# Optimization experiments

Hardware: AMD Instinct MI355X
Metric: run time of the kernel (lower is better)

Reference implementation:

```python
import jax, jax.numpy as jnp
import numpy as np

NUM_HEADS = 16
GROUP_SIZE = 4
RMS_EPS = 1e-6


def _rope_cos_sin(S, head_dim):
    # matches compute_freqs_cis: freqs = 1/10000**(arange(0,hd,2)/hd), angles = outer(t, freqs)
    inv_freq = 1.0 / (10000.0 ** (jnp.arange(0, head_dim, 2, dtype=jnp.float32) / head_dim))
    t = jnp.arange(S, dtype=jnp.float32)
    angles = t[:, None] * inv_freq[None, :]          # [S, hd/2]
    return jnp.cos(angles), jnp.sin(angles)


def _apply_rope(x, cos, sin):
    # x: [B, S, h, hd]; complex multiply on (even, odd) pairs
    B, S, h, hd = x.shape
    xr = x.reshape(B, S, h, hd // 2, 2)
    x0, x1 = xr[..., 0], xr[..., 1]
    c = cos[None, :, None, :]
    s = sin[None, :, None, :]
    o0 = x0 * c - x1 * s
    o1 = x0 * s + x1 * c
    return jnp.stack([o0, o1], axis=-1).reshape(B, S, h, hd)


def setup_inputs() -> dict:
    key = jax.random.key(0)
    k1, k2, k3 = jax.random.split(key, 3)
    B, S, H = 4, 2048, 2048
    g = GROUP_SIZE
    x = jax.random.normal(k1, (B, S, H), dtype=jnp.float32)
    w_attn = jax.random.normal(k2, (H, H + 2 * H // g), dtype=jnp.float32) * 0.02
    w_proj = jax.random.normal(k3, (H, H), dtype=jnp.float32) * 0.02
    norm_w = jnp.ones((H,), dtype=jnp.float32)
    return {"x": x, "w_attn": w_attn, "w_proj": w_proj, "norm_w": norm_w}


def reference(x, w_attn, w_proj, norm_w):
    B, S, H = x.shape
    nh = NUM_HEADS
    g = GROUP_SIZE
    nkv = nh // g
    hd = H // nh
    ghd = H // g

    qkv = jnp.einsum('bsh,hf->bsf', x, w_attn)
    q = qkv[..., :H].reshape(B, S, nh, hd)
    k = qkv[..., H:H + ghd].reshape(B, S, nkv, hd)
    v = qkv[..., H + ghd:].reshape(B, S, nkv, hd)

    cos, sin = _rope_cos_sin(S, hd)
    q = _apply_rope(q, cos, sin)
    k = _apply_rope(k, cos, sin)

    q = q.transpose(0, 2, 1, 3)                      # [B, nh, S, hd]
    k = jnp.repeat(k.transpose(0, 2, 1, 3), g, axis=1)   # [B, nh, S, hd]
    v = jnp.repeat(v.transpose(0, 2, 1, 3), g, axis=1)

    scale = 1.0 / jnp.sqrt(jnp.float32(hd))
    scores = jnp.einsum('bhqd,bhkd->bhqk', q, k) * scale
    causal = jnp.tril(jnp.ones((S, S), dtype=bool))
    scores = jnp.where(causal[None, None], scores, jnp.finfo(scores.dtype).min)
    attn = jax.nn.softmax(scores, axis=-1)
    y = jnp.einsum('bhqk,bhkd->bhqd', attn, v)       # [B, nh, S, hd]
    y = y.transpose(0, 2, 1, 3).reshape(B, S, H)

    y = jnp.einsum('bsh,ho->bso', y, w_proj)
    # RMSNorm
    rms = jnp.sqrt(jnp.mean(jnp.square(y), axis=-1, keepdims=True) + RMS_EPS)
    return (y / rms) * norm_w
```

## Files before the change

kernel.cpp:

```cpp
#include <hip/hip_runtime.h>

#define DEVI __device__ __forceinline__

using u16 = unsigned short;
using u32 = unsigned int;

typedef __attribute__((ext_vector_type(8))) short short8v;
typedef __attribute__((ext_vector_type(4))) float f32x4;
typedef __attribute__((ext_vector_type(2))) u32 u32x2;

DEVI u16 f2b(float f) {
  u32 u = __builtin_bit_cast(u32, f);
  u += 0x7fffu + ((u >> 16) & 1u);
  return (u16)(u >> 16);
}
DEVI float b2f(u16 b) { return __builtin_bit_cast(float, (u32)b << 16); }

DEVI void gload16(const void* g, void* l) {
  __builtin_amdgcn_global_load_lds(
      (const __attribute__((address_space(1))) void*)g,
      (__attribute__((address_space(3))) void*)l, 16, 0, 0);
}

__global__ __launch_bounds__(256) void cvt_x_k(const float* __restrict__ in,
                                               u16* __restrict__ out) {
  size_t i = ((size_t)blockIdx.x * 256 + threadIdx.x) * 8;
  f32x4 a = *(const f32x4*)(in + i);
  f32x4 c = *(const f32x4*)(in + i + 4);
  short8v o;
  o[0] = (short)f2b(a[0]); o[1] = (short)f2b(a[1]);
  o[2] = (short)f2b(a[2]); o[3] = (short)f2b(a[3]);
  o[4] = (short)f2b(c[0]); o[5] = (short)f2b(c[1]);
  o[6] = (short)f2b(c[2]); o[7] = (short)f2b(c[3]);
  *(short8v*)(out + i) = o;
}

__global__ __launch_bounds__(256) void transpose_cvt_k(
    const float* __restrict__ in, u16* __restrict__ out, int R, int Ccols) {
  __shared__ u16 tile[64][65];
  const int r0 = blockIdx.y * 64, c0 = blockIdx.x * 64;
  const int tx = threadIdx.x & 63, ty = threadIdx.x >> 6;
#pragma unroll
  for (int jj = 0; jj < 16; ++jj) {
    int r = ty + jj * 4;
    tile[r][tx] = f2b(in[(size_t)(r0 + r) * Ccols + c0 + tx]);
  }
  __syncthreads();
#pragma unroll
  for (int jj = 0; jj < 16; ++jj) {
    int c = ty + jj * 4;
    out[(size_t)(c0 + c) * R + r0 + tx] = tile[tx][c];
  }
}

__global__ __launch_bounds__(256) void rope_table_k(float* __restrict__ cosT,
                                                    float* __restrict__ sinT) {
  int idx = blockIdx.x * 256 + threadIdx.x;
  int s = idx >> 6, i = idx & 63;
  float inv_freq = expf(-(float)i * (1.0f / 64.0f) * 9.210340371976184f);
  float ang = (float)s * inv_freq;
  cosT[idx] = cosf(ang);
  sinT[idx] = sinf(ang);
}

__global__ __launch_bounds__(256) void rope_scatter_k(
    const u16* __restrict__ qkv, const float* __restrict__ cosT,
    const float* __restrict__ sinT, u16* __restrict__ q_r,
    u16* __restrict__ k_r) {
  const float QS = 0.08838834764831845f * 1.4426950408889634f;
  const int row = blockIdx.x;
  const int b = row >> 11, s = row & 2047;
  const u16* in = qkv + (size_t)row * 3072;
  const float* cp = cosT + s * 64;
  const float* sp = sinT + s * 64;
  for (int p = threadIdx.x; p < 1280; p += 256) {
    int f0 = p * 2;
    u32 pair = *(const u32*)(in + f0);
    float x0 = b2f((u16)(pair & 0xffffu));
    float x1 = b2f((u16)(pair >> 16));
    int d, head;
    u16* dst;
    bool isq = (f0 < 2048);
    if (isq) {
      head = f0 >> 7; d = f0 & 127;
      dst = q_r + (((size_t)(b * 16 + head)) * 2048 + s) * 128 + d;
    } else {
      int idx = f0 - 2048;
      head = idx >> 7; d = idx & 127;
      dst = k_r + (((size_t)(b * 4 + head)) * 2048 + s) * 128 + d;
    }
    int i = d >> 1;
    float c = cp[i], sn = sp[i];
    float o0 = x0 * c - x1 * sn;
    float o1 = x0 * sn + x1 * c;
    if (isq) { o0 *= QS; o1 *= QS; }
    *(u32*)dst = (u32)f2b(o0) | ((u32)f2b(o1) << 16);
  }
}

__global__ __launch_bounds__(256) void v_trans_k(const u16* __restrict__ qkv,
                                                 u16* __restrict__ vT) {
  __shared__ u16 tile[64][65];
  const int s0 = blockIdx.x * 64, d0 = blockIdx.y * 64;
  const int bk = blockIdx.z;
  const int b = bk >> 2, kh = bk & 3;
  const int tx = threadIdx.x & 63, ty = threadIdx.x >> 6;
  const u16* src = qkv + ((size_t)b * 2048) * 3072 + 2560 + kh * 128;
#pragma unroll
  for (int jj = 0; jj < 16; ++jj) {
    int s = ty + jj * 4;
    tile[s][tx] = src[(size_t)(s0 + s) * 3072 + d0 + tx];
  }
  __syncthreads();
  u16* dst = vT + (((size_t)bk * 128 + d0) * 2048) + s0;
#pragma unroll
  for (int jj = 0; jj < 16; ++jj) {
    int dd = ty + jj * 4;
    dst[(size_t)dd * 2048 + tx] = tile[tx][dd];
  }
}

DEVI short8v ldf(const char* half, int r, int slot) {
  return *(const short8v*)(half + r * 64 + (((slot) ^ (r & 3)) << 4));
}

DEVI void stg(const u16* __restrict__ G, int row0, int Kd, int T, int kh,
              char* dst, int t, int w) {
#pragma unroll
  for (int i = 0; i < 2; ++i) {
    int off = i * 8192 + t * 16;
    int r = off >> 6;
    int gs = ((off >> 4) & 3) ^ (r & 3);
    gload16((const char*)G +
                (((size_t)(row0 + r) * Kd) + T * 64 + kh * 32 + gs * 8) * 2,
            dst + i * 8192 + w * 1024);
  }
}

#define VM4 asm volatile("s_waitcnt vmcnt(4)" ::: "memory")
#define PH(P2, KS, CH, STAGE_STMT, TAILWAIT)                                   \
  {                                                                            \
    if ((CH) == 0) {                                                           \
      _Pragma("unroll") for (int mt = 0; mt < 8; ++mt) af[mt] =                \
          ldf(Ab + (P2) * 32768 + (KS) * 16384, wm * 128 + mt * 16 + lo, hi);  \
    }                                                                          \
    bf0 = ldf(Bb + (P2) * 32768 + (KS) * 16384, wn * 64 + (CH) * 32 + lo, hi);\
    bf1 = ldf(Bb + (P2) * 32768 + (KS) * 16384,                                \
              wn * 64 + (CH) * 32 + 16 + lo, hi);                              \
    STAGE_STMT;                                                                \
    __builtin_amdgcn_sched_barrier(0);                                         \
    __builtin_amdgcn_s_barrier();                                              \
    asm volatile("s_waitcnt lgkmcnt(0)" ::: "memory");                         \
    __builtin_amdgcn_sched_barrier(0);                                         \
    __builtin_amdgcn_s_setprio(1);                                             \
    _Pragma("unroll") for (int mt = 0; mt < 8; ++mt) {                         \
      acc[mt][(CH) * 2] = __builtin_amdgcn_mfma_f32_16x16x32_bf16(             \
          af[mt], bf0, acc[mt][(CH) * 2], 0, 0, 0);                            \
      acc[mt][(CH) * 2 + 1] = __builtin_amdgcn_mfma_f32_16x16x32_bf16(         \
          af[mt], bf1, acc[mt][(CH) * 2 + 1], 0, 0, 0);                        \
    }                                                                          \
    __builtin_amdgcn_s_setprio(0);                                             \
    TAILWAIT;                                                                  \
    __builtin_amdgcn_sched_barrier(0);                                         \
    __builtin_amdgcn_s_barrier();                                              \
    __builtin_amdgcn_sched_barrier(0);                                         \
  }

__global__ __launch_bounds__(512, 2) void gemm256_k(const u16* __restrict__ A,
                                                    const u16* __restrict__ BT,
                                                    u16* __restrict__ C, int N,
                                                    int Kd) {
  __shared__ __align__(16) char lds[131072];
  char* Ab = lds;
  char* Bb = lds + 65536;

  const int t = threadIdx.x;
  const int lane = t & 63, lo = lane & 15, hi = lane >> 4;
  const int w = t >> 6, wm = w >> 2, wn = w & 3;

  const int ntx = gridDim.x;
  const int nwg = ntx * gridDim.y;
  const int orig = blockIdx.y * ntx + blockIdx.x;
  const int cpx = nwg >> 3;
  const int swz = (orig & 7) * cpx + (orig >> 3);
  const int m0 = (swz / ntx) * 256, n0 = (swz % ntx) * 256;

  f32x4 acc[8][4];
#pragma unroll
  for (int a = 0; a < 8; ++a)
#pragma unroll
    for (int c = 0; c < 4; ++c) acc[a][c] = (f32x4){0.f, 0.f, 0.f, 0.f};

  short8v af[8], bf0, bf1;

  const int NK = Kd >> 6;
  const int NK2 = NK >> 1;

  stg(A, m0, Kd, 0, 0, Ab + 0, t, w);
  stg(BT, n0, Kd, 0, 0, Bb + 0, t, w);
  stg(A, m0, Kd, 0, 1, Ab + 16384, t, w);
  stg(BT, n0, Kd, 0, 1, Bb + 16384, t, w);
  stg(A, m0, Kd, 1, 0, Ab + 32768, t, w);
  stg(BT, n0, Kd, 1, 0, Bb + 32768, t, w);
  VM4;
  __builtin_amdgcn_sched_barrier(0);
  __builtin_amdgcn_s_barrier();
  __builtin_amdgcn_sched_barrier(0);

  for (int kt2 = 0; kt2 < NK2; ++kt2) {
    int T1v = 2 * kt2 + 1;
    int T2v = 2 * kt2 + 2; if (T2v > NK - 1) T2v = NK - 1;
    int T3v = 2 * kt2 + 3; if (T3v > NK - 1) T3v = NK - 1;
    PH(0, 0, 0, stg(A, m0, Kd, T1v, 1, Ab + 49152, t, w), (void)0);
    PH(0, 0, 1, stg(BT, n0, Kd, T1v, 1, Bb + 49152, t, w), (void)0);
    PH(0, 1, 0, stg(A, m0, Kd, T2v, 0, Ab + 0, t, w), (void)0);
    PH(0, 1, 1, stg(BT, n0, Kd, T2v, 0, Bb + 0, t, w), VM4);
    PH(1, 0, 0, stg(A, m0, Kd, T2v, 1, Ab + 16384, t, w), (void)0);
    PH(1, 0, 1, stg(BT, n0, Kd, T2v, 1, Bb + 16384, t, w), (void)0);
    PH(1, 1, 0, stg(A, m0, Kd, T3v, 0, Ab + 32768, t, w), (void)0);
    PH(1, 1, 1, stg(BT, n0, Kd, T3v, 0, Bb + 32768, t, w), VM4);
  }
  asm volatile("s_waitcnt vmcnt(0)" ::: "memory");

#pragma unroll
  for (int mt = 0; mt < 8; ++mt)
#pragma unroll
    for (int nt = 0; nt < 4; ++nt)
#pragma unroll
      for (int r = 0; r < 4; ++r) {
        int row = m0 + wm * 128 + mt * 16 + hi * 4 + r;
        int col = n0 + wn * 64 + nt * 16 + lo;
        C[(size_t)row * N + col] = f2b(acc[mt][nt][r]);
      }
}

__global__ __launch_bounds__(256, 3) void attn_k(const u16* __restrict__ Q,
                                                 const u16* __restrict__ K,
                                                 const u16* __restrict__ VT,
                                                 u16* __restrict__ Y) {
  __shared__ __align__(16) u16 lK[2][32 * 128];
  __shared__ __align__(16) u16 lV[2][128 * 32];
  __shared__ __align__(16) u16 lP[4][32 * 32];

  const int t = threadIdx.x;
  const int lane = t & 63, lo = lane & 15, hi = lane >> 4;
  const int w = t >> 6;

  const int id = blockIdx.x;
  const int xcd = id & 7, pos = id >> 3;
  const int bh = xcd + ((pos >> 4) << 3);
  const int qt = 15 - (pos & 15);
  const int b = bh >> 4, h = bh & 15, kh = h >> 2;

  const size_t qbase = (size_t)(b * 16 + h) * 2048 * 128;
  const size_t kbase = (size_t)(b * 4 + kh) * 2048 * 128;
  const size_t vbase = (size_t)(b * 4 + kh) * 128 * 2048;

  const int q0 = qt * 128;
  const int wq0 = q0 + w * 32;

  short8v qf[2][4];
#pragma unroll
  for (int j2 = 0; j2 < 2; ++j2)
#pragma unroll
    for (int ks = 0; ks < 4; ++ks)
      qf[j2][ks] = *(const short8v*)(Q + qbase +
                                     (size_t)(wq0 + j2 * 16 + lo) * 128 +
                                     ks * 32 + hi * 8);

  float m_run[2], l_run[2];
  m_run[0] = -3.0e38f; m_run[1] = -3.0e38f;
  l_run[0] = 0.f; l_run[1] = 0.f;
  f32x4 oacc[2][8];
#pragma unroll
  for (int j2 = 0; j2 < 2; ++j2)
#pragma unroll
    for (int ot = 0; ot < 8; ++ot) oacc[j2][ot] = (f32x4){0.f, 0.f, 0.f, 0.f};

  const int ntile = 4 * qt + 4;

  auto stage = [&](int buf, int j) {
    const int kv0 = j * 32;
#pragma unroll
    for (int i = 0; i < 2; ++i) {
      int off = i * 4096 + t * 16;
      int r = off >> 8;
      int sl = (off >> 4) & 15;
      int gs = sl ^ (r & 7);
      gload16((const char*)K + (kbase + (size_t)(kv0 + r) * 128 + gs * 8) * 2,
              (char*)lK[buf] + i * 4096 + w * 1024);
    }
#pragma unroll
    for (int i = 0; i < 2; ++i) {
      int off = i * 4096 + t * 16;
      int r = off >> 6;
      int sl = (off >> 4) & 3;
      int gs = sl ^ (r & 3);
      gload16((const char*)VT + (vbase + (size_t)r * 2048 + kv0 + gs * 8) * 2,
              (char*)lV[buf] + i * 4096 + w * 1024);
    }
  };

  stage(0, 0);
  __syncthreads();

  u16* pw = lP[w];

  for (int jj = 0; jj < ntile; ++jj) {
    const int cur = jj & 1;
    if (jj + 1 < ntile) stage(cur ^ 1, jj + 1);

    const u16* lKc = lK[cur];
    const u16* lVc = lV[cur];
    const int kv0 = jj * 32;

    f32x4 sacc[2][2];
#pragma unroll
    for (int j2 = 0; j2 < 2; ++j2)
#pragma unroll
      for (int kt = 0; kt < 2; ++kt) sacc[j2][kt] = (f32x4){0.f, 0.f, 0.f, 0.f};
    __builtin_amdgcn_s_setprio(1);
#pragma unroll
    for (int ks = 0; ks < 4; ++ks) {
#pragma unroll
      for (int kt = 0; kt < 2; ++kt) {
        int kr = kt * 16 + lo;
        int sl = (ks * 4 + hi) ^ (kr & 7);
        short8v kf = *(const short8v*)((const char*)lKc + kr * 256 + (sl << 4));
        sacc[0][kt] = __builtin_amdgcn_mfma_f32_16x16x32_bf16(kf, qf[0][ks],
                                                              sacc[0][kt], 0, 0, 0);
        sacc[1][kt] = __builtin_amdgcn_mfma_f32_16x16x32_bf16(kf, qf[1][ks],
                                                              sacc[1][kt], 0, 0, 0);
      }
    }
    __builtin_amdgcn_s_setprio(0);

    if (jj >= ntile - 4) {
      const int kb = kv0 + hi * 4 - wq0 - lo;
#pragma unroll
      for (int j2 = 0; j2 < 2; ++j2)
#pragma unroll
        for (int kt = 0; kt < 2; ++kt)
#pragma unroll
          for (int r = 0; r < 4; ++r)
            if (kb + kt * 16 + r - j2 * 16 > 0) sacc[j2][kt][r] = -1.0e38f;
    }

    float pmax[2];
#pragma unroll
    for (int j2 = 0; j2 < 2; ++j2) {
      f32x4 m4;
#pragma unroll
      for (int r = 0; r < 4; ++r) m4[r] = fmaxf(sacc[j2][0][r], sacc[j2][1][r]);
      float m = fmaxf(fmaxf(m4[0], m4[1]), fmaxf(m4[2], m4[3]));
      m = fmaxf(m, __shfl_xor(m, 16, 64));
      m = fmaxf(m, __shfl_xor(m, 32, 64));
      pmax[j2] = m;
    }

    bool need = (pmax[0] > m_run[0] + 8.f) || (pmax[1] > m_run[1] + 8.f);
    if (__any(need)) {
      float corr[2];
#pragma unroll
      for (int j2 = 0; j2 < 2; ++j2) {
        float mn = fmaxf(m_run[j2], pmax[j2]);
        corr[j2] = exp2f(m_run[j2] - mn);
        m_run[j2] = mn;
        l_run[j2] *= corr[j2];
      }
#pragma unroll
      for (int j2 = 0; j2 < 2; ++j2) {
        float c0 = __shfl(corr[j2], hi * 4 + 0, 64);
        float c1 = __shfl(corr[j2], hi * 4 + 1, 64);
        float c2 = __shfl(corr[j2], hi * 4 + 2, 64);
        float c3 = __shfl(corr[j2], hi * 4 + 3, 64);
#pragma unroll
        for (int ot = 0; ot < 8; ++ot) {
          oacc[j2][ot][0] *= c0;
          oacc[j2][ot][1] *= c1;
          oacc[j2][ot][2] *= c2;
          oacc[j2][ot][3] *= c3;
        }
      }
    }

#pragma unroll
    for (int j2 = 0; j2 < 2; ++j2) {
      const float rowm = m_run[j2];
      float s0 = 0.f, s1 = 0.f, s2 = 0.f, s3 = 0.f;
#pragma unroll
      for (int kt = 0; kt < 2; ++kt) {
        float p0 = exp2f(sacc[j2][kt][0] - rowm);
        float p1 = exp2f(sacc[j2][kt][1] - rowm);
        float p2 = exp2f(sacc[j2][kt][2] - rowm);
        float p3 = exp2f(sacc[j2][kt][3] - rowm);
        s0 += p0; s1 += p1; s2 += p2; s3 += p3;
        u32 w0, w1;
        asm("v_cvt_pk_bf16_f32 %0, %1, %2" : "=v"(w0) : "v"(p0), "v"(p1));
        asm("v_cvt_pk_bf16_f32 %0, %1, %2" : "=v"(w1) : "v"(p2), "v"(p3));
        int byte = ((((kt * 2 + (hi >> 1)) ^ (lo & 3)) << 4) | ((hi & 1) << 3));
        *(u32x2*)((char*)pw + (j2 * 16 + lo) * 64 + byte) = (u32x2){w0, w1};
      }
      float sm = (s0 + s1) + (s2 + s3);
      sm += __shfl_xor(sm, 16, 64);
      sm += __shfl_xor(sm, 32, 64);
      l_run[j2] += sm;
    }

    __builtin_amdgcn_s_setprio(1);
    {
      short8v pa0 = *(const short8v*)((const char*)pw + lo * 64 +
                                      ((hi ^ (lo & 3)) << 4));
      short8v pa1 = *(const short8v*)((const char*)pw + (16 + lo) * 64 +
                                      ((hi ^ (lo & 3)) << 4));
#pragma unroll
      for (int ot = 0; ot < 8; ++ot) {
        int vr = ot * 16 + lo;
        int sl = hi ^ (vr & 3);
        short8v vf = *(const short8v*)((const char*)lVc + vr * 64 + (sl << 4));
        oacc[0][ot] =
            __builtin_amdgcn_mfma_f32_16x16x32_bf16(pa0, vf, oacc[0][ot], 0, 0, 0);
        oacc[1][ot] =
            __builtin_amdgcn_mfma_f32_16x16x32_bf16(pa1, vf, oacc[1][ot], 0, 0, 0);
      }
    }
    __builtin_amdgcn_s_setprio(0);

    __syncthreads();
  }

  float inv[2][4];
#pragma unroll
  for (int j2 = 0; j2 < 2; ++j2)
#pragma unroll
    for (int r = 0; r < 4; ++r) {
      float lv = __shfl(l_run[j2], hi * 4 + r, 64);
      inv[j2][r] = 1.0f / lv;
    }
#pragma unroll
  for (int j2 = 0; j2 < 2; ++j2)
#pragma unroll
    for (int ot = 0; ot < 8; ++ot)
#pragma unroll
      for (int r = 0; r < 4; ++r) {
        int qrow = wq0 + j2 * 16 + hi * 4 + r;
        Y[((size_t)b * 2048 + qrow) * 2048 + h * 128 + ot * 16 + lo] =
            f2b(oacc[j2][ot][r] * inv[j2][r]);
      }
}

__global__ __launch_bounds__(256) void rmsnorm_k(const u16* __restrict__ Yb,
                                                 const float* __restrict__ nw,
                                                 float* __restrict__ out) {
  const int row = blockIdx.x;
  const int t = threadIdx.x;
  const u16* yr = Yb + (size_t)row * 2048 + t * 8;
  short8v v = *(const short8v*)yr;
  float x[8];
  float ss = 0.f;
#pragma unroll
  for (int j = 0; j < 8; ++j) {
    x[j] = b2f((u16)v[j]);
    ss += x[j] * x[j];
  }
#pragma unroll
  for (int dm = 1; dm < 64; dm <<= 1) ss += __shfl_xor(ss, dm, 64);
  __shared__ float red[4];
  if ((t & 63) == 0) red[t >> 6] = ss;
  __syncthreads();
  float tot = red[0] + red[1] + red[2] + red[3];
  float inv = rsqrtf(tot * (1.0f / 2048.0f) + 1e-6f);
  float* op = out + (size_t)row * 2048 + t * 8;
  const float* wp = nw + t * 8;
  f32x4 o0, o1;
#pragma unroll
  for (int j = 0; j < 4; ++j) o0[j] = x[j] * inv * wp[j];
#pragma unroll
  for (int j = 0; j < 4; ++j) o1[j] = x[4 + j] * inv * wp[4 + j];
  *(f32x4*)op = o0;
  *(f32x4*)(op + 4) = o1;
}

extern "C" void kernel_launch(void* const* d_in, const int* in_sizes, int n_in,
                              void* d_out, int out_size, void* d_ws,
                              size_t ws_size, hipStream_t stream) {
  (void)in_sizes; (void)n_in; (void)out_size; (void)ws_size;
  const float* x = (const float*)d_in[0];
  const float* w_attn = (const float*)d_in[1];
  const float* w_proj = (const float*)d_in[2];
  const float* norm_w = (const float*)d_in[3];
  float* out = (float*)d_out;
  char* ws = (char*)d_ws;

  size_t off = 0;
  auto alloc = [&](size_t n) {
    size_t r = off;
    off += (n + 255) & ~(size_t)255;
    return r;
  };
  u16* xb = (u16*)(ws + alloc(33554432));
  u16* wabT = (u16*)(ws + alloc(12582912));
  u16* qkv = (u16*)(ws + alloc(50331648));
  u16* q_r = (u16*)(ws + alloc(33554432));
  u16* vT = (u16*)(ws + alloc(8388608));
  u16* wpT = (u16*)(ws + alloc(8388608));
  float* cosT = (float*)(ws + alloc(524288));
  float* sinT = (float*)(ws + alloc(524288));
  u16* k_r = wabT;
  u16* y = xb;
  u16* y2 = qkv;

  cvt_x_k<<<8192, 256, 0, stream>>>(x, xb);
  transpose_cvt_k<<<dim3(48, 32), 256, 0, stream>>>(w_attn, wabT, 2048, 3072);
  transpose_cvt_k<<<dim3(32, 32), 256, 0, stream>>>(w_proj, wpT, 2048, 2048);
  rope_table_k<<<512, 256, 0, stream>>>(cosT, sinT);
  gemm256_k<<<dim3(12, 32), 512, 0, stream>>>(xb, wabT, qkv, 3072, 2048);
  rope_scatter_k<<<8192, 256, 0, stream>>>(qkv, cosT, sinT, q_r, k_r);
  v_trans_k<<<dim3(32, 2, 16), 256, 0, stream>>>(qkv, vT);
  attn_k<<<dim3(1024), 256, 0, stream>>>(q_r, k_r, vT, y);
  gemm256_k<<<dim3(8, 32), 512, 0, stream>>>(y, wpT, y2, 2048, 2048);
  rmsnorm_k<<<8192, 256, 0, stream>>>(y2, norm_w, out);
}
```

Baseline: 428.1 us.

## Rewrite attention with 32x32 MFMA, 64-wide KV tiles, register-resident P

```diff
diff --git a/kernel.cpp b/kernel.cpp
--- a/kernel.cpp
+++ b/kernel.cpp
@@ -7,7 +7,9 @@
 
 typedef __attribute__((ext_vector_type(8))) short short8v;
 typedef __attribute__((ext_vector_type(4))) float f32x4;
+typedef __attribute__((ext_vector_type(16))) float f32x16;
 typedef __attribute__((ext_vector_type(2))) u32 u32x2;
+typedef __attribute__((ext_vector_type(4))) u32 u32x4;
 
 DEVI u16 f2b(float f) {
   u32 u = __builtin_bit_cast(u32, f);
@@ -234,16 +236,16 @@
       }
 }
 
-__global__ __launch_bounds__(256, 3) void attn_k(const u16* __restrict__ Q,
+__global__ __launch_bounds__(256, 2) void attn_k(const u16* __restrict__ Q,
                                                  const u16* __restrict__ K,
                                                  const u16* __restrict__ VT,
                                                  u16* __restrict__ Y) {
-  __shared__ __align__(16) u16 lK[2][32 * 128];
-  __shared__ __align__(16) u16 lV[2][128 * 32];
-  __shared__ __align__(16) u16 lP[4][32 * 32];
+  __shared__ __align__(16) u16 lK[2][64 * 128];
+  __shared__ __align__(16) u16 lV[2][128 * 64];
 
   const int t = threadIdx.x;
-  const int lane = t & 63, lo = lane & 15, hi = lane >> 4;
+  const int lane = t & 63;
+  const int l31 = lane & 31, hb = lane >> 5;
   const int w = t >> 6;
 
   const int id = blockIdx.x;
@@ -257,32 +259,26 @@
   const size_t vbase = (size_t)(b * 4 + kh) * 128 * 2048;
 
   const int q0 = qt * 128;
-  const int wq0 = q0 + w * 32;
-
-  short8v qf[2][4];
-#pragma unroll
-  for (int j2 = 0; j2 < 2; ++j2)
-#pragma unroll
-    for (int ks = 0; ks < 4; ++ks)
-      qf[j2][ks] = *(const short8v*)(Q + qbase +
-                                     (size_t)(wq0 + j2 * 16 + lo) * 128 +
-                                     ks * 32 + hi * 8);
-
-  float m_run[2], l_run[2];
-  m_run[0] = -3.0e38f; m_run[1] = -3.0e38f;
-  l_run[0] = 0.f; l_run[1] = 0.f;
-  f32x4 oacc[2][8];
-#pragma unroll
-  for (int j2 = 0; j2 < 2; ++j2)
-#pragma unroll
-    for (int ot = 0; ot < 8; ++ot) oacc[j2][ot] = (f32x4){0.f, 0.f, 0.f, 0.f};
-
-  const int ntile = 4 * qt + 4;
+  const int qrow = q0 + w * 32 + l31;
+
+  short8v qf[8];
+#pragma unroll
+  for (int j16 = 0; j16 < 8; ++j16)
+    qf[j16] = *(const short8v*)(Q + qbase + (size_t)qrow * 128 + j16 * 16 + hb * 8);
+
+  float m_run = -3.0e38f, l_run = 0.f;
+  f32x16 oacc[4];
+#pragma unroll
+  for (int db = 0; db < 4; ++db)
+#pragma unroll
+    for (int rg = 0; rg < 16; ++rg) oacc[db][rg] = 0.f;
+
+  const int ntile = 2 * qt + 2;
 
   auto stage = [&](int buf, int j) {
-    const int kv0 = j * 32;
-#pragma unroll
-    for (int i = 0; i < 2; ++i) {
+    const int kv0 = j * 64;
+#pragma unroll
+    for (int i = 0; i < 4; ++i) {
       int off = i * 4096 + t * 16;
       int r = off >> 8;
       int sl = (off >> 4) & 15;
@@ -291,11 +287,11 @@
               (char*)lK[buf] + i * 4096 + w * 1024);
     }
 #pragma unroll
-    for (int i = 0; i < 2; ++i) {
+    for (int i = 0; i < 4; ++i) {
       int off = i * 4096 + t * 16;
-      int r = off >> 6;
-      int sl = (off >> 4) & 3;
-      int gs = sl ^ (r & 3);
+      int r = off >> 7;
+      int sl = (off >> 4) & 7;
+      int gs = sl ^ (r & 7);
       gload16((const char*)VT + (vbase + (size_t)r * 2048 + kv0 + gs * 8) * 2,
               (char*)lV[buf] + i * 4096 + w * 1024);
     }
@@ -303,150 +299,127 @@
 
   stage(0, 0);
   __syncthreads();
-
-  u16* pw = lP[w];
 
   for (int jj = 0; jj < ntile; ++jj) {
     const int cur = jj & 1;
     if (jj + 1 < ntile) stage(cur ^ 1, jj + 1);
 
-    const u16* lKc = lK[cur];
-    const u16* lVc = lV[cur];
-    const int kv0 = jj * 32;
-
-    f32x4 sacc[2][2];
-#pragma unroll
-    for (int j2 = 0; j2 < 2; ++j2)
-#pragma unroll
-      for (int kt = 0; kt < 2; ++kt) sacc[j2][kt] = (f32x4){0.f, 0.f, 0.f, 0.f};
+    const char* lKc = (const char*)lK[cur];
+    const char* lVc = (const char*)lV[cur];
+    const int kv0 = jj * 64;
+
+    f32x16 sacc[2];
+#pragma unroll
+    for (int kb = 0; kb < 2; ++kb)
+#pragma unroll
+      for (int rg = 0; rg < 16; ++rg) sacc[kb][rg] = 0.f;
+
     __builtin_amdgcn_s_setprio(1);
 #pragma unroll
-    for (int ks = 0; ks < 4; ++ks) {
-#pragma unroll
-      for (int kt = 0; kt < 2; ++kt) {
-        int kr = kt * 16 + lo;
-        int sl = (ks * 4 + hi) ^ (kr & 7);
-        short8v kf = *(const short8v*)((const char*)lKc + kr * 256 + (sl << 4));
-        sacc[0][kt] = __builtin_amdgcn_mfma_f32_16x16x32_bf16(kf, qf[0][ks],
-                                                              sacc[0][kt], 0, 0, 0);
-        sacc[1][kt] = __builtin_amdgcn_mfma_f32_16x16x32_bf16(kf, qf[1][ks],
-                                                              sacc[1][kt], 0, 0, 0);
+    for (int j16 = 0; j16 < 8; ++j16) {
+      const int c = j16 * 2 + hb;
+#pragma unroll
+      for (int kb = 0; kb < 2; ++kb) {
+        int kr = kb * 32 + l31;
+        short8v kf = *(const short8v*)(lKc + kr * 256 + ((c ^ (kr & 7)) << 4));
+        sacc[kb] = __builtin_amdgcn_mfma_f32_32x32x16_bf16(kf, qf[j16],
+                                                           sacc[kb], 0, 0, 0);
       }
     }
     __builtin_amdgcn_s_setprio(0);
 
-    if (jj >= ntile - 4) {
-      const int kb = kv0 + hi * 4 - wq0 - lo;
-#pragma unroll
-      for (int j2 = 0; j2 < 2; ++j2)
-#pragma unroll
-        for (int kt = 0; kt < 2; ++kt)
-#pragma unroll
-          for (int r = 0; r < 4; ++r)
-            if (kb + kt * 16 + r - j2 * 16 > 0) sacc[j2][kt][r] = -1.0e38f;
-    }
-
-    float pmax[2];
-#pragma unroll
-    for (int j2 = 0; j2 < 2; ++j2) {
-      f32x4 m4;
-#pragma unroll
-      for (int r = 0; r < 4; ++r) m4[r] = fmaxf(sacc[j2][0][r], sacc[j2][1][r]);
-      float m = fmaxf(fmaxf(m4[0], m4[1]), fmaxf(m4[2], m4[3]));
-      m = fmaxf(m, __shfl_xor(m, 16, 64));
-      m = fmaxf(m, __shfl_xor(m, 32, 64));
-      pmax[j2] = m;
-    }
-
-    bool need = (pmax[0] > m_run[0] + 8.f) || (pmax[1] > m_run[1] + 8.f);
-    if (__any(need)) {
-      float corr[2];
-#pragma unroll
-      for (int j2 = 0; j2 < 2; ++j2) {
-        float mn = fmaxf(m_run[j2], pmax[j2]);
-        corr[j2] = exp2f(m_run[j2] - mn);
-        m_run[j2] = mn;
-        l_run[j2] *= corr[j2];
+    if (jj >= ntile - 2) {
+      const int mb = kv0 + 4 * hb - qrow;
+#pragma unroll
+      for (int kb = 0; kb < 2; ++kb)
+#pragma unroll
+        for (int rg = 0; rg < 16; ++rg)
+          if (mb + kb * 32 + (rg & 3) + 8 * (rg >> 2) > 0)
+            sacc[kb][rg] = -1.0e38f;
+    }
+
+    float mx = sacc[0][0];
+#pragma unroll
+    for (int rg = 1; rg < 16; ++rg) mx = fmaxf(mx, sacc[0][rg]);
+#pragma unroll
+    for (int rg = 0; rg < 16; ++rg) mx = fmaxf(mx, sacc[1][rg]);
+    mx = fmaxf(mx, __shfl_xor(mx, 32, 64));
+
+    if (__any(mx > m_run + 8.f)) {
+      float mn = fmaxf(m_run, mx);
+      float corr = exp2f(m_run - mn);
+      m_run = mn;
+      l_run *= corr;
+#pragma unroll
+      for (int db = 0; db < 4; ++db)
+#pragma unroll
+        for (int rg = 0; rg < 16; ++rg) oacc[db][rg] *= corr;
+    }
+
+    float sm = 0.f;
+#pragma unroll
+    for (int kb = 0; kb < 2; ++kb)
+#pragma unroll
+      for (int rg = 0; rg < 16; ++rg) {
+        float p = exp2f(sacc[kb][rg] - m_run);
+        sacc[kb][rg] = p;
+        sm += p;
       }
-#pragma unroll
-      for (int j2 = 0; j2 < 2; ++j2) {
-        float c0 = __shfl(corr[j2], hi * 4 + 0, 64);
-        float c1 = __shfl(corr[j2], hi * 4 + 1, 64);
-        float c2 = __shfl(corr[j2], hi * 4 + 2, 64);
-        float c3 = __shfl(corr[j2], hi * 4 + 3, 64);
-#pragma unroll
-        for (int ot = 0; ot < 8; ++ot) {
-          oacc[j2][ot][0] *= c0;
-          oacc[j2][ot][1] *= c1;
-          oacc[j2][ot][2] *= c2;
-          oacc[j2][ot][3] *= c3;
-        }
+    sm += __shfl_xor(sm, 32, 64);
+    l_run += sm;
+
+    short8v pa[4];
+#pragma unroll
+    for (int kb = 0; kb < 2; ++kb) {
+      u32 pw00, pw01, pw10, pw11, pw20, pw21, pw30, pw31;
+      asm("v_cvt_pk_bf16_f32 %0, %1, %2" : "=v"(pw00) : "v"(sacc[kb][0]), "v"(sacc[kb][1]));
+      asm("v_cvt_pk_bf16_f32 %0, %1, %2" : "=v"(pw01) : "v"(sacc[kb][2]), "v"(sacc[kb][3]));
+      asm("v_cvt_pk_bf16_f32 %0, %1, %2" : "=v"(pw10) : "v"(sacc[kb][4]), "v"(sacc[kb][5]));
+      asm("v_cvt_pk_bf16_f32 %0, %1, %2" : "=v"(pw11) : "v"(sacc[kb][6]), "v"(sacc[kb][7]));
+      asm("v_cvt_pk_bf16_f32 %0, %1, %2" : "=v"(pw20) : "v"(sacc[kb][8]), "v"(sacc[kb][9]));
+      asm("v_cvt_pk_bf16_f32 %0, %1, %2" : "=v"(pw21) : "v"(sacc[kb][10]), "v"(sacc[kb][11]));
+      asm("v_cvt_pk_bf16_f32 %0, %1, %2" : "=v"(pw30) : "v"(sacc[kb][12]), "v"(sacc[kb][13]));
+      asm("v_cvt_pk_bf16_f32 %0, %1, %2" : "=v"(pw31) : "v"(sacc[kb][14]), "v"(sacc[kb][15]));
+      u32x2 a0 = __builtin_amdgcn_permlane32_swap(pw00, pw10, false, false);
+      u32x2 a1 = __builtin_amdgcn_permlane32_swap(pw01, pw11, false, false);
+      u32x4 wv0; wv0[0] = a0[0]; wv0[1] = a1[0]; wv0[2] = a0[1]; wv0[3] = a1[1];
+      pa[kb * 2 + 0] = __builtin_bit_cast(short8v, wv0);
+      u32x2 b0 = __builtin_amdgcn_permlane32_swap(pw20, pw30, false, false);
+      u32x2 b1 = __builtin_amdgcn_permlane32_swap(pw21, pw31, false, false);
+      u32x4 wv1; wv1[0] = b0[0]; wv1[1] = b1[0]; wv1[2] = b0[1]; wv1[3] = b1[1];
+      pa[kb * 2 + 1] = __builtin_bit_cast(short8v, wv1);
+    }
+
+    __builtin_amdgcn_s_setprio(1);
+#pragma unroll
+    for (int sc = 0; sc < 4; ++sc) {
+      const int c = sc * 2 + hb;
+#pragma unroll
+      for (int db = 0; db < 4; ++db) {
+        int vr = db * 32 + l31;
+        short8v vf = *(const short8v*)(lVc + vr * 128 + ((c ^ (vr & 7)) << 4));
+        oacc[db] = __builtin_amdgcn_mfma_f32_32x32x16_bf16(vf, pa[sc],
+                                                           oacc[db], 0, 0, 0);
       }
     }
-
-#pragma unroll
-    for (int j2 = 0; j2 < 2; ++j2) {
-      const float rowm = m_run[j2];
-      float s0 = 0.f, s1 = 0.f, s2 = 0.f, s3 = 0.f;
-#pragma unroll
-      for (int kt = 0; kt < 2; ++kt) {
-        float p0 = exp2f(sacc[j2][kt][0] - rowm);
-        float p1 = exp2f(sacc[j2][kt][1] - rowm);
-        float p2 = exp2f(sacc[j2][kt][2] - rowm);
-        float p3 = exp2f(sacc[j2][kt][3] - rowm);
-        s0 += p0; s1 += p1; s2 += p2; s3 += p3;
-        u32 w0, w1;
-        asm("v_cvt_pk_bf16_f32 %0, %1, %2" : "=v"(w0) : "v"(p0), "v"(p1));
-        asm("v_cvt_pk_bf16_f32 %0, %1, %2" : "=v"(w1) : "v"(p2), "v"(p3));
-        int byte = ((((kt * 2 + (hi >> 1)) ^ (lo & 3)) << 4) | ((hi & 1) << 3));
-        *(u32x2*)((char*)pw + (j2 * 16 + lo) * 64 + byte) = (u32x2){w0, w1};
-      }
-      float sm = (s0 + s1) + (s2 + s3);
-      sm += __shfl_xor(sm, 16, 64);
-      sm += __shfl_xor(sm, 32, 64);
-      l_run[j2] += sm;
-    }
-
-    __builtin_amdgcn_s_setprio(1);
-    {
-      short8v pa0 = *(const short8v*)((const char*)pw + lo * 64 +
-                                      ((hi ^ (lo & 3)) << 4));
-      short8v pa1 = *(const short8v*)((const char*)pw + (16 + lo) * 64 +
-                                      ((hi ^ (lo & 3)) << 4));
-#pragma unroll
-      for (int ot = 0; ot < 8; ++ot) {
-        int vr = ot * 16 + lo;
-        int sl = hi ^ (vr & 3);
-        short8v vf = *(const short8v*)((const char*)lVc + vr * 64 + (sl << 4));
-        oacc[0][ot] =
-            __builtin_amdgcn_mfma_f32_16x16x32_bf16(pa0, vf, oacc[0][ot], 0, 0, 0);
-        oacc[1][ot] =
-            __builtin_amdgcn_mfma_f32_16x16x32_bf16(pa1, vf, oacc[1][ot], 0, 0, 0);
-      }
-    }
     __builtin_amdgcn_s_setprio(0);
 
     __syncthreads();
   }
 
-  float inv[2][4];
-#pragma unroll
-  for (int j2 = 0; j2 < 2; ++j2)
-#pragma unroll
-    for (int r = 0; r < 4; ++r) {
-      float lv = __shfl(l_run[j2], hi * 4 + r, 64);
-      inv[j2][r] = 1.0f / lv;
-    }
-#pragma unroll
-  for (int j2 = 0; j2 < 2; ++j2)
-#pragma unroll
-    for (int ot = 0; ot < 8; ++ot)
-#pragma unroll
-      for (int r = 0; r < 4; ++r) {
-        int qrow = wq0 + j2 * 16 + hi * 4 + r;
-        Y[((size_t)b * 2048 + qrow) * 2048 + h * 128 + ot * 16 + lo] =
-            f2b(oacc[j2][ot][r] * inv[j2][r]);
-      }
+  const float inv = 1.0f / l_run;
+  u16* yp = Y + ((size_t)b * 2048 + qrow) * 2048 + h * 128;
+#pragma unroll
+  for (int db = 0; db < 4; ++db)
+#pragma unroll
+    for (int j = 0; j < 4; ++j) {
+      float a0 = oacc[db][4 * j] * inv, a1 = oacc[db][4 * j + 1] * inv;
+      float a2 = oacc[db][4 * j + 2] * inv, a3 = oacc[db][4 * j + 3] * inv;
+      u32 w0, w1;
+      asm("v_cvt_pk_bf16_f32 %0, %1, %2" : "=v"(w0) : "v"(a0), "v"(a1));
+      asm("v_cvt_pk_bf16_f32 %0, %1, %2" : "=v"(w1) : "v"(a2), "v"(a3));
+      *(u32x2*)(yp + db * 32 + 8 * j + 4 * hb) = (u32x2){w0, w1};
+    }
 }
 
 __global__ __launch_bounds__(256) void rmsnorm_k(const u16* __restrict__ Yb,
```

Result: faster. 404.5 us (-5.5%).
